# Optimization experiments

Hardware: AMD Instinct MI355X
Metric: run time of the kernel (lower is better)

Reference implementation:

```python
import jax, jax.numpy as jnp
import numpy as np
import math

H = 2048      # hidden_size
NH = 32       # num heads
HD = H // NH  # head_dim = 64
THETA = 10000.0
B, S = 2, 2048


def _rope_tables(seq_len):
    inv_freq = 1.0 / (THETA ** (jnp.arange(0, HD, 2, dtype=jnp.float32) / HD))
    t = jnp.arange(seq_len, dtype=jnp.float32)
    freqs = t[:, None] * inv_freq[None, :]          # [S, HD/2]
    emb = jnp.concatenate([freqs, freqs], axis=-1)  # [S, HD]
    return jnp.cos(emb)[None, None], jnp.sin(emb)[None, None]  # [1,1,S,HD]


def _rotate_half(x):
    x1, x2 = jnp.split(x, 2, axis=-1)
    return jnp.concatenate([-x2, x1], axis=-1)


def setup_inputs() -> dict:
    key = jax.random.key(0)
    ks = jax.random.split(key, 5)
    hidden_states = jax.random.normal(ks[0], (B, S, H), dtype=jnp.float32)
    wscale = 1.0 / math.sqrt(H)
    wq = jax.random.normal(ks[1], (H, H), dtype=jnp.float32) * wscale
    wk = jax.random.normal(ks[2], (H, H), dtype=jnp.float32) * wscale
    wv = jax.random.normal(ks[3], (H, H), dtype=jnp.float32) * wscale
    wo = jax.random.normal(ks[4], (H, H), dtype=jnp.float32) * wscale
    # additive causal mask: 0 on/below diagonal, -1e9 above
    causal = jnp.tril(jnp.ones((S, S), dtype=bool))
    attention_mask = jnp.where(causal, 0.0, -1e9).astype(jnp.float32)[None, None]
    return {"hidden_states": hidden_states, "attention_mask": attention_mask,
            "wq": wq, "wk": wk, "wv": wv, "wo": wo}


def reference(hidden_states, attention_mask, wq, wk, wv, wo):
    b, s, _ = hidden_states.shape
    # projections (Linear, no bias); weights stored [in, out]
    q = (hidden_states @ wq).reshape(b, s, NH, HD).transpose(0, 2, 1, 3)  # [B,NH,S,HD]
    k = (hidden_states @ wk).reshape(b, s, NH, HD).transpose(0, 2, 1, 3)
    v = (hidden_states @ wv).reshape(b, s, NH, HD).transpose(0, 2, 1, 3)
    # RoPE
    cos, sin = _rope_tables(s)
    q = q * cos + _rotate_half(q) * sin
    k = k * cos + _rotate_half(k) * sin
    # attention
    attn = jnp.einsum('bhqd,bhkd->bhqk', q, k) / math.sqrt(HD)
    attn = attn + attention_mask
    w = jax.nn.softmax(attn, axis=-1)
    out = jnp.einsum('bhqk,bhkd->bhqd', w, v)           # [B,NH,S,HD]
    out = out.transpose(0, 2, 1, 3).reshape(b, s, H)    # [B,S,H]
    return out @ wo
```

## Files before the change

### kernel.cpp

```cpp
#include <hip/hip_runtime.h>
#include <hip/hip_bf16.h>

#define H 2048
#define NH 32
#define HD 64
#define BB 2
#define SS 2048
#define MM (BB*SS)

typedef __attribute__((ext_vector_type(8))) short bf16x8;
typedef __attribute__((ext_vector_type(4))) float f32x4;
typedef __attribute__((ext_vector_type(16))) float f32x16;
typedef unsigned short u16;
typedef unsigned int u32;
typedef __attribute__((ext_vector_type(4))) u32 u32x4;

#define MFMA16(acc, av, bv) acc = __builtin_amdgcn_mfma_f32_16x16x32_bf16(av, bv, acc, 0, 0, 0)

static __device__ __forceinline__ u16 f2bf(float f){
  union { float f; u32 i; } v; v.f = f;
  u32 x = v.i;
  return (u16)((x + 0x7FFFu + ((x >> 16) & 1u)) >> 16);
}
static __device__ __forceinline__ float bf2f(u16 u){
  union { u32 i; float f; } v; v.i = ((u32)u) << 16; return v.f;
}
static __device__ __forceinline__ u32 pk2(float a, float b){
  u32 r;
  asm("v_cvt_pk_bf16_f32 %0, %1, %2" : "=v"(r) : "v"(a), "v"(b));
  return r;
}

static __device__ __forceinline__ void gload16(const u16* g, u16* l){
  __builtin_amdgcn_global_load_lds((const __attribute__((address_space(1))) void*)g,
                                   (__attribute__((address_space(3))) void*)l, 16, 0, 0);
}

__global__ void k_cvt(const float* __restrict__ src, u16* __restrict__ dst){
  const int i = (blockIdx.x * 256 + threadIdx.x) * 4;
  float4 v = *(const float4*)(src + i);
  ushort4 o;
  o.x = f2bf(v.x); o.y = f2bf(v.y); o.z = f2bf(v.z); o.w = f2bf(v.w);
  *(ushort4*)(dst + i) = o;
}

__global__ void k_wtrans(const float* __restrict__ w0, const float* __restrict__ w1,
                         const float* __restrict__ w2, const float* __restrict__ w3,
                         u16* __restrict__ d0, u16* __restrict__ d1,
                         u16* __restrict__ d2, u16* __restrict__ d3){
  __shared__ float tile[32][33];
  const int z = blockIdx.z;
  const float* w = z==0 ? w0 : z==1 ? w1 : z==2 ? w2 : w3;
  u16* d        = z==0 ? d0 : z==1 ? d1 : z==2 ? d2 : d3;
  const int n0 = blockIdx.x * 32, k0 = blockIdx.y * 32;
  const int tx = threadIdx.x, ty = threadIdx.y;
  #pragma unroll
  for (int j = 0; j < 4; j++)
    tile[ty + 8*j][tx] = w[(size_t)(k0 + ty + 8*j) * H + n0 + tx];
  __syncthreads();
  #pragma unroll
  for (int j = 0; j < 4; j++)
    d[(size_t)(n0 + ty + 8*j) * H + k0 + tx] = f2bf(tile[tx][ty + 8*j]);
}

__global__ __launch_bounds__(512, 4) void k_gemm8(
    const u16* __restrict__ A, const u16* __restrict__ Bt,
    u16* __restrict__ CQ, u16* __restrict__ CK, u16* __restrict__ CV,
    int M, int K){
  __shared__ __align__(16) u16 As[2][128][64];
  __shared__ __align__(16) u16 Bs[2][192][64];
  const int flat = blockIdx.x;
  const int id = (flat & 7) * 128 + (flat >> 3);
  const int gy = id >> 5, gx = id & 31;
  const int m0 = gx * 128, n0 = gy * 192;
  const int t = threadIdx.x, w = t >> 6, l = t & 63;
  const int wm = w >> 2, wn = w & 3;
  const int lrow = l & 15, lk = (l >> 4) * 8;
  const int sw = (lrow & 7) * 8;
  const int sr = t >> 3, sc = (t & 7) * 8;
  const int ssc = sc ^ ((sr & 7) * 8);
  const int NK = K >> 6;

  auto stageA = [&](int kt, int u){
    const size_t kb = (size_t)kt * 64 + ssc;
    #pragma unroll
    for (int c = 0; c < 2; c++)
      gload16(A + (size_t)(m0 + c*64 + sr) * K + kb, &As[u][c*64 + sr][sc]);
  };
  auto stageB = [&](int kt, int u){
    const size_t kb = (size_t)kt * 64 + ssc;
    #pragma unroll
    for (int c = 0; c < 3; c++)
      gload16(Bt + (size_t)(n0 + c*64 + sr) * K + kb, &Bs[u][c*64 + sr][sc]);
  };

  f32x4 acc[4][3] = {};

  stageA(0, 0); stageB(0, 0);
  stageA(1, 1); stageB(1, 1);
  asm volatile("s_waitcnt vmcnt(5)" ::: "memory");
  __builtin_amdgcn_s_barrier();

  #pragma unroll 1
  for (int kt = 0; kt < NK; ++kt){
    const int u = kt & 1;
    const bool more = (kt + 2 < NK);
    bf16x8 b0[3], b1[3], a0, a1;

    #pragma unroll
    for (int n = 0; n < 3; n++)
      b0[n] = *(const bf16x8*)&Bs[u][wn*48 + n*16 + lrow][lk ^ sw];
    a0 = *(const bf16x8*)&As[u][wm*64 +  0 + lrow][lk ^ sw];
    a1 = *(const bf16x8*)&As[u][wm*64 + 16 + lrow][lk ^ sw];
    __builtin_amdgcn_s_setprio(1);
    #pragma unroll
    for (int n = 0; n < 3; n++){
      MFMA16(acc[0][n], a0, b0[n]);
      MFMA16(acc[1][n], a1, b0[n]);
    }
    __builtin_amdgcn_s_setprio(0);
    __builtin_amdgcn_s_barrier();

    #pragma unroll
    for (int n = 0; n < 3; n++)
      b1[n] = *(const bf16x8*)&Bs[u][wn*48 + n*16 + lrow][(32 + lk) ^ sw];
    a0 = *(const bf16x8*)&As[u][wm*64 +  0 + lrow][(32 + lk) ^ sw];
    a1 = *(const bf16x8*)&As[u][wm*64 + 16 + lrow][(32 + lk) ^ sw];
    __builtin_amdgcn_s_setprio(1);
    #pragma unroll
    for (int n = 0; n < 3; n++){
      MFMA16(acc[0][n], a0, b1[n]);
      MFMA16(acc[1][n], a1, b1[n]);
    }
    __builtin_amdgcn_s_setprio(0);
    __builtin_amdgcn_s_barrier();

    if (more) stageB(kt + 2, u);
    a0 = *(const bf16x8*)&As[u][wm*64 + 32 + lrow][lk ^ sw];
    a1 = *(const bf16x8*)&As[u][wm*64 + 48 + lrow][lk ^ sw];
    __builtin_amdgcn_s_setprio(1);
    #pragma unroll
    for (int n = 0; n < 3; n++){
      MFMA16(acc[2][n], a0, b0[n]);
      MFMA16(acc[3][n], a1, b0[n]);
    }
    __builtin_amdgcn_s_setprio(0);
    __builtin_amdgcn_s_barrier();

    a0 = *(const bf16x8*)&As[u][wm*64 + 32 + lrow][(32 + lk) ^ sw];
    a1 = *(const bf16x8*)&As[u][wm*64 + 48 + lrow][(32 + lk) ^ sw];
    __builtin_amdgcn_s_setprio(1);
    #pragma unroll
    for (int n = 0; n < 3; n++){
      MFMA16(acc[2][n], a0, b1[n]);
      MFMA16(acc[3][n], a1, b1[n]);
    }
    __builtin_amdgcn_s_setprio(0);
    __builtin_amdgcn_s_barrier();

    if (more){
      stageA(kt + 2, u);
      asm volatile("s_waitcnt vmcnt(5)" ::: "memory");
      __builtin_amdgcn_s_barrier();
    } else if (kt + 1 < NK){
      asm volatile("s_waitcnt vmcnt(0)" ::: "memory");
      __builtin_amdgcn_s_barrier();
    }
  }

  #pragma unroll
  for (int m = 0; m < 4; m++)
    #pragma unroll
    for (int n = 0; n < 3; n++){
      const int ncol = n0 + wn*48 + n*16 + lrow;
      const int z = ncol >> 11;
      u16* C = (z == 0 ? CQ : z == 1 ? CK : CV) + (ncol & 2047);
      #pragma unroll
      for (int r = 0; r < 4; r++){
        const int row = m0 + wm*64 + m*16 + (l >> 4)*4 + r;
        C[(size_t)row * H] = f2bf(acc[m][n][r]);
      }
    }
}

__global__ __launch_bounds__(512, 4) void k_gemmo(
    const u16* __restrict__ A, const u16* __restrict__ Bt,
    float* __restrict__ C, int M, int N, int K){
  __shared__ __align__(16) u16 As[2][128][64];
  __shared__ __align__(16) u16 Bs[2][128][64];
  const int flat = blockIdx.x;
  const int id = (flat & 7) * 64 + (flat >> 3);
  const int gy = id >> 5, gx = id & 31;
  const int m0 = gx * 128, n0 = gy * 128;
  const int t = threadIdx.x, w = t >> 6, l = t & 63;
  const int wm = w >> 2, wn = w & 3;
  const int lrow = l & 15, lk = (l >> 4) * 8;
  const int sw = (lrow & 7) * 8;
  const int sr = t >> 3, sc = (t & 7) * 8;
  const int ssc = sc ^ ((sr & 7) * 8);
  const int NK = K >> 6;

  auto stageA = [&](int kt, int u){
    const size_t kb = (size_t)kt * 64 + ssc;
    #pragma unroll
    for (int c = 0; c < 2; c++)
      gload16(A + (size_t)(m0 + c*64 + sr) * K + kb, &As[u][c*64 + sr][sc]);
  };
  auto stageB = [&](int kt, int u){
    const size_t kb = (size_t)kt * 64 + ssc;
    #pragma unroll
    for (int c = 0; c < 2; c++)
      gload16(Bt + (size_t)(n0 + c*64 + sr) * K + kb, &Bs[u][c*64 + sr][sc]);
  };

  f32x4 acc[4][2] = {};

  stageA(0, 0); stageB(0, 0);
  stageA(1, 1); stageB(1, 1);
  asm volatile("s_waitcnt vmcnt(4)" ::: "memory");
  __builtin_amdgcn_s_barrier();

  #pragma unroll 1
  for (int kt = 0; kt < NK; ++kt){
    const int u = kt & 1;
    const bool more = (kt + 2 < NK);
    bf16x8 b0[2], b1[2], a0, a1;

    #pragma unroll
    for (int n = 0; n < 2; n++)
      b0[n] = *(const bf16x8*)&Bs[u][wn*32 + n*16 + lrow][lk ^ sw];
    a0 = *(const bf16x8*)&As[u][wm*64 +  0 + lrow][lk ^ sw];
    a1 = *(const bf16x8*)&As[u][wm*64 + 16 + lrow][lk ^ sw];
    __builtin_amdgcn_s_setprio(1);
    #pragma unroll
    for (int n = 0; n < 2; n++){
      MFMA16(acc[0][n], a0, b0[n]);
      MFMA16(acc[1][n], a1, b0[n]);
    }
    __builtin_amdgcn_s_setprio(0);
    __builtin_amdgcn_s_barrier();

    #pragma unroll
    for (int n = 0; n < 2; n++)
      b1[n] = *(const bf16x8*)&Bs[u][wn*32 + n*16 + lrow][(32 + lk) ^ sw];
    a0 = *(const bf16x8*)&As[u][wm*64 +  0 + lrow][(32 + lk) ^ sw];
    a1 = *(const bf16x8*)&As[u][wm*64 + 16 + lrow][(32 + lk) ^ sw];
    __builtin_amdgcn_s_setprio(1);
    #pragma unroll
    for (int n = 0; n < 2; n++){
      MFMA16(acc[0][n], a0, b1[n]);
      MFMA16(acc[1][n], a1, b1[n]);
    }
    __builtin_amdgcn_s_setprio(0);
    __builtin_amdgcn_s_barrier();

    if (more) stageB(kt + 2, u);
    a0 = *(const bf16x8*)&As[u][wm*64 + 32 + lrow][lk ^ sw];
    a1 = *(const bf16x8*)&As[u][wm*64 + 48 + lrow][lk ^ sw];
    __builtin_amdgcn_s_setprio(1);
    #pragma unroll
    for (int n = 0; n < 2; n++){
      MFMA16(acc[2][n], a0, b0[n]);
      MFMA16(acc[3][n], a1, b0[n]);
    }
    __builtin_amdgcn_s_setprio(0);
    __builtin_amdgcn_s_barrier();

    a0 = *(const bf16x8*)&As[u][wm*64 + 32 + lrow][(32 + lk) ^ sw];
    a1 = *(const bf16x8*)&As[u][wm*64 + 48 + lrow][(32 + lk) ^ sw];
    __builtin_amdgcn_s_setprio(1);
    #pragma unroll
    for (int n = 0; n < 2; n++){
      MFMA16(acc[2][n], a0, b1[n]);
      MFMA16(acc[3][n], a1, b1[n]);
    }
    __builtin_amdgcn_s_setprio(0);
    __builtin_amdgcn_s_barrier();

    if (more){
      stageA(kt + 2, u);
      asm volatile("s_waitcnt vmcnt(4)" ::: "memory");
      __builtin_amdgcn_s_barrier();
    } else if (kt + 1 < NK){
      asm volatile("s_waitcnt vmcnt(0)" ::: "memory");
      __builtin_amdgcn_s_barrier();
    }
  }

  #pragma unroll
  for (int m = 0; m < 4; m++)
    #pragma unroll
    for (int n = 0; n < 2; n++){
      const int col = n0 + wn*32 + n*16 + lrow;
      #pragma unroll
      for (int r = 0; r < 4; r++){
        const int row = m0 + wm*64 + m*16 + (l >> 4)*4 + r;
        C[(size_t)row * N + col] = acc[m][n][r];
      }
    }
}

__global__ void k_rope(u16* __restrict__ Kp){
  const int idx = blockIdx.x * 256 + threadIdx.x;
  const int quad = idx & 3;
  const int h = (idx >> 2) & 31;
  const int row = idx >> 7;
  const int s = row & (SS - 1);
  const int i0 = quad * 8;
  u16* k = Kp + (size_t)row * H + h * HD;
  uint4 k1v = *(const uint4*)(k + i0);
  uint4 k2v = *(const uint4*)(k + i0 + 32);
  u16* k1 = (u16*)&k1v; u16* k2 = (u16*)&k2v;
  const float sf = (float)s;
  #pragma unroll
  for (int e = 0; e < 8; e++){
    const int i = i0 + e;
    const float inv = exp2f(-0.4152410118609203f * (float)i);
    float rev = sf * inv * 0.15915494309189535f;
    rev -= floorf(rev);
    const float sn = __builtin_amdgcn_sinf(rev);
    const float cs = __builtin_amdgcn_cosf(rev);
    const float ka = bf2f(k1[e]), kb = bf2f(k2[e]);
    k1[e] = f2bf(ka*cs - kb*sn);
    k2[e] = f2bf(kb*cs + ka*sn);
  }
  *(uint4*)(k + i0)      = k1v;
  *(uint4*)(k + i0 + 32) = k2v;
}

__global__ __launch_bounds__(256, 2) void k_attn(
    const u16* __restrict__ Q, const u16* __restrict__ K,
    const u16* __restrict__ V, u16* __restrict__ O){
  __shared__ __align__(16) u16 Ks[3][64][64];
  __shared__ __align__(16) u16 Vs[2][64][72];
  const int t = threadIdx.x, w = t >> 6, l = t & 63;
  const int x = blockIdx.x, bh = blockIdx.y;
  const int b = bh >> 5, h = bh & 31;
  const u16* kp = K + (size_t)(b*SS) * H + h * HD;
  const u16* vp = V + (size_t)(b*SS) * H + h * HD;
  const int sr = t >> 3, sc = (t & 7) * 8;
  const int ssc = sc ^ ((sr & 7) * 8);
  const int hi = l >> 5, lq = l & 31;
  const float QSC = 0.18033688011112042f;

  auto stageK = [&](int tile, int buf){
    const int jb = tile * 64;
    gload16(kp + (size_t)(jb + sr) * H + ssc,      &Ks[buf][sr][sc]);
    gload16(kp + (size_t)(jb + 32 + sr) * H + ssc, &Ks[buf][32 + sr][sc]);
  };
  auto loadV = [&](int tile, uint4* vv){
    const int jb = tile * 64;
    vv[0] = *(const uint4*)(vp + (size_t)(jb + sr) * H + sc);
    vv[1] = *(const uint4*)(vp + (size_t)(jb + 32 + sr) * H + sc);
  };
  auto publishV = [&](const uint4* vv, int buf){
    #pragma unroll
    for (int c = 0; c < 2; c++){
      const int j = c*32 + sr;
      const u16* pv = (const u16*)&vv[c];
      #pragma unroll
      for (int e = 0; e < 8; e++){
        const int d = sc + e;
        Vs[buf][d][j ^ ((d >> 3) * 8)] = pv[e];
      }
    }
  };

  #pragma unroll 1
  for (int pp = 0; pp < 2; pp++){
    const int qt = pp ? x : (15 - x);
    const int NT = 2*qt + 2;
    const int qw0 = qt*128 + w*32;
    const int qrow = qw0 + lq;

    const u16* qptr = Q + (size_t)(b*SS + qrow) * H + h * HD + hi*8;
    bf16x8 qr0 = *(const bf16x8*)(qptr + 0);
    bf16x8 qr1 = *(const bf16x8*)(qptr + 16);
    bf16x8 qr2 = *(const bf16x8*)(qptr + 32);
    bf16x8 qr3 = *(const bf16x8*)(qptr + 48);
    bf16x8 qf[4];
    {
      const float sf = (float)qrow;
      #pragma unroll
      for (int e = 0; e < 8; e++){
        #pragma unroll
        for (int pr = 0; pr < 2; pr++){
          const int d = pr*16 + hi*8 + e;
          const float inv = exp2f(-0.4152410118609203f * (float)d);
          float rev = sf * inv * 0.15915494309189535f;
          rev -= floorf(rev);
          const float sn = __builtin_amdgcn_sinf(rev);
          const float cs = __builtin_amdgcn_cosf(rev);
          const float qa = bf2f((u16)(pr ? qr1[e] : qr0[e]));
          const float qb = bf2f((u16)(pr ? qr3[e] : qr2[e]));
          const u16 oa = f2bf((qa*cs - qb*sn) * QSC);
          const u16 ob = f2bf((qb*cs + qa*sn) * QSC);
          if (pr){ qf[1][e] = (short)oa; qf[3][e] = (short)ob; }
          else   { qf[0][e] = (short)oa; qf[2][e] = (short)ob; }
        }
      }
    }

    float mrun = -1e30f, lrun = 0.f;
    f32x16 oacc[2] = {};
    uint4 vvE[2], vvO[2];

    stageK(0, 0); loadV(0, vvE);
    stageK(1, 1); loadV(1, vvO);
    asm volatile("s_waitcnt vmcnt(4)" ::: "memory");
    publishV(vvE, 0);
    asm volatile("s_waitcnt lgkmcnt(0)" ::: "memory");
    __builtin_amdgcn_s_barrier();

    auto body = [&](int jt, int p, uint4* vvSelf, const uint4* vvOther){
      const int j0 = jt * 64;
      if (jt + 2 < NT){ stageK(jt + 2, (jt + 2) % 3); loadV(jt + 2, vvSelf); }

      if (j0 <= qw0){
        const int kbuf = jt % 3;
        f32x16 sv[2] = {};
        __builtin_amdgcn_s_setprio(1);
        #pragma unroll
        for (int kb = 0; kb < 2; kb++){
          const int row = kb*32 + lq;
          #pragma unroll
          for (int c = 0; c < 4; c++){
            bf16x8 kf = *(const bf16x8*)&Ks[kbuf][row][(c*16 + hi*8) ^ ((row & 7) * 8)];
            sv[kb] = __builtin_amdgcn_mfma_f32_32x32x16_bf16(kf, qf[c], sv[kb], 0, 0, 0);
          }
        }
        __builtin_amdgcn_s_setprio(0);
        if (j0 + 63 > qw0){
          #pragma unroll
          for (int kb = 0; kb < 2; kb++)
            #pragma unroll
            for (int r = 0; r < 16; r++){
              const int kg = j0 + kb*32 + (r & 3) + 8*(r >> 2) + 4*hi;
              if (kg > qrow) sv[kb][r] = -1e30f;
            }
        }
        float t16[16], t8[8], t4[4];
        #pragma unroll
        for (int r = 0; r < 16; r++) t16[r] = fmaxf(sv[0][r], sv[1][r]);
        #pragma unroll
        for (int r = 0; r < 8; r++) t8[r] = fmaxf(t16[r], t16[r+8]);
        #pragma unroll
        for (int r = 0; r < 4; r++) t4[r] = fmaxf(t8[r], t8[r+4]);
        float tm = fmaxf(fmaxf(t4[0], t4[2]), fmaxf(t4[1], t4[3]));
        tm = fmaxf(tm, __shfl_xor(tm, 32, 64));
        if (__any(tm > mrun)){
          const float mn = fmaxf(mrun, tm);
          const float fac = exp2f(mrun - mn);
          mrun = mn;
          lrun *= fac;
          #pragma unroll
          for (int db = 0; db < 2; db++)
            #pragma unroll
            for (int r = 0; r < 16; r++) oacc[db][r] *= fac;
        }
        #pragma unroll
        for (int kb = 0; kb < 2; kb++)
          #pragma unroll
          for (int r = 0; r < 16; r++) sv[kb][r] = exp2f(sv[kb][r] - mrun);
        float s16[16], s8[8], s4[4];
        #pragma unroll
        for (int r = 0; r < 16; r++) s16[r] = sv[0][r] + sv[1][r];
        #pragma unroll
        for (int r = 0; r < 8; r++) s8[r] = s16[r] + s16[r+8];
        #pragma unroll
        for (int r = 0; r < 4; r++) s4[r] = s8[r] + s8[r+4];
        float rs = (s4[0] + s4[1]) + (s4[2] + s4[3]);
        rs += __shfl_xor(rs, 32, 64);
        lrun += rs;
        u32x4 pw[4];
        #pragma unroll
        for (int kb = 0; kb < 2; kb++){
          #pragma unroll
          for (int half = 0; half < 2; half++){
            const int rb = half * 8;
            const u32 own0 = pk2(sv[kb][rb+0], sv[kb][rb+1]);
            const u32 own1 = pk2(sv[kb][rb+2], sv[kb][rb+3]);
            const u32 own2 = pk2(sv[kb][rb+4], sv[kb][rb+5]);
            const u32 own3 = pk2(sv[kb][rb+6], sv[kb][rb+7]);
            const u32 s0 = hi ? own0 : own2;
            const u32 s1 = hi ? own1 : own3;
            const u32 r0 = __shfl_xor(s0, 32, 64);
            const u32 r1 = __shfl_xor(s1, 32, 64);
            u32x4 pv;
            pv[0] = hi ? r0 : own0;
            pv[1] = hi ? r1 : own1;
            pv[2] = hi ? own2 : r0;
            pv[3] = hi ? own3 : r1;
            pw[kb*2 + half] = pv;
          }
        }
        __builtin_amdgcn_s_setprio(1);
        #pragma unroll
        for (int db = 0; db < 2; db++){
          const int d = db*32 + lq;
          #pragma unroll
          for (int tt = 0; tt < 4; tt++){
            bf16x8 vf = *(const bf16x8*)&Vs[p][d][(tt*16 + hi*8) ^ ((d >> 3) * 8)];
            bf16x8 pfr = __builtin_bit_cast(bf16x8, pw[tt]);
            oacc[db] = __builtin_amdgcn_mfma_f32_32x32x16_bf16(vf, pfr, oacc[db], 0, 0, 0);
          }
        }
        __builtin_amdgcn_s_setprio(0);
      }

      if (jt + 2 < NT) asm volatile("s_waitcnt vmcnt(4)" ::: "memory");
      else             asm volatile("s_waitcnt vmcnt(0)" ::: "memory");
      if (jt + 1 < NT) publishV(vvOther, p ^ 1);
      asm volatile("s_waitcnt lgkmcnt(0)" ::: "memory");
      __builtin_amdgcn_s_barrier();
    };

    #pragma unroll 1
    for (int jt2 = 0; jt2 < NT; jt2 += 2){
      body(jt2,     0, vvE, vvO);
      body(jt2 + 1, 1, vvO, vvE);
    }

    const float rl = 1.0f / lrun;
    u16* op = O + (size_t)(b*SS + qrow) * H + h * HD;
    #pragma unroll
    for (int db = 0; db < 2; db++)
      #pragma unroll
      for (int rq = 0; rq < 4; rq++){
        ushort4 o4;
        o4.x = f2bf(oacc[db][rq*4 + 0] * rl);
        o4.y = f2bf(oacc[db][rq*4 + 1] * rl);
        o4.z = f2bf(oacc[db][rq*4 + 2] * rl);
        o4.w = f2bf(oacc[db][rq*4 + 3] * rl);
        *(ushort4*)(op + db*32 + rq*8 + 4*hi) = o4;
      }
  }
}

extern "C" void kernel_launch(void* const* d_in, const int* in_sizes, int n_in,
                              void* d_out, int out_size, void* d_ws, size_t ws_size,
                              hipStream_t stream){
  (void)in_sizes; (void)n_in; (void)out_size; (void)ws_size;
  const float* hs = (const float*)d_in[0];
  const float* wq = (const float*)d_in[2];
  const float* wk = (const float*)d_in[3];
  const float* wv = (const float*)d_in[4];
  const float* wo = (const float*)d_in[5];
  float* out = (float*)d_out;
  char* ws = (char*)d_ws;

  u16* Xb  = (u16*)ws;
  u16* Wqt = (u16*)(ws + (size_t)MM * H * 2);
  u16* Wkt = Wqt + (size_t)H * H;
  u16* Wvt = Wkt + (size_t)H * H;
  u16* Wot = Wvt + (size_t)H * H;
  u16* Vb  = Wot + (size_t)H * H;
  u16* Ob  = Vb  + (size_t)MM * H;
  u16* Qb  = (u16*)d_out;
  u16* Kb  = Qb + (size_t)MM * H;

  k_cvt<<<8192, 256, 0, stream>>>(hs, Xb);
  k_wtrans<<<dim3(64, 64, 4), dim3(32, 8), 0, stream>>>(wq, wk, wv, wo, Wqt, Wkt, Wvt, Wot);
  k_gemm8<<<1024, 512, 0, stream>>>(Xb, Wqt, Qb, Kb, Vb, MM, H);
  k_rope<<<2048, 256, 0, stream>>>(Kb);
  k_attn<<<dim3(8, 64), 256, 0, stream>>>(Qb, Kb, Vb, Ob);
  k_gemmo<<<512, 512, 0, stream>>>(Ob, Wot, out, MM, H, H);
}
```

Baseline: 278.0 us.

## Process two KV tiles per barrier with 4-deep K/V buffers and lazy rescale

Restructures the attention main loop to stage and compute two key/value tiles per iteration, using four shared-memory buffers for both K and V. This halves the number of barriers and waitcnt points per tile. It also raises the online-softmax rescale threshold so the output accumulator is only rescaled when the max grows by a margin, and defers the cross-half row-sum shuffle to the end. In exchange shared-memory use rises, which may hurt occupancy at 2 blocks per CU, and the lazy max risks a precision change.

Result: no change. 273.1 us, median of 2 (-1.8%).

```diff
diff --git a/kernel.cpp b/kernel.cpp
--- a/kernel.cpp
+++ b/kernel.cpp
@@ -331,8 +331,8 @@
 __global__ __launch_bounds__(256, 2) void k_attn(
     const u16* __restrict__ Q, const u16* __restrict__ K,
     const u16* __restrict__ V, u16* __restrict__ O){
-  __shared__ __align__(16) u16 Ks[3][64][64];
-  __shared__ __align__(16) u16 Vs[2][64][72];
+  __shared__ __align__(16) u16 Ks[4][64][64];
+  __shared__ __align__(16) u16 Vs[4][64][72];
   const int t = threadIdx.x, w = t >> 6, l = t & 63;
   const int x = blockIdx.x, bh = blockIdx.y;
   const int b = bh >> 5, h = bh & 31;
@@ -403,124 +403,127 @@
 
     float mrun = -1e30f, lrun = 0.f;
     f32x16 oacc[2] = {};
-    uint4 vvE[2], vvO[2];
-
-    stageK(0, 0); loadV(0, vvE);
-    stageK(1, 1); loadV(1, vvO);
-    asm volatile("s_waitcnt vmcnt(4)" ::: "memory");
-    publishV(vvE, 0);
+    uint4 vvA[2], vvB[2];
+
+    stageK(0, 0); loadV(0, vvA);
+    stageK(1, 1); loadV(1, vvB);
+    asm volatile("s_waitcnt vmcnt(0)" ::: "memory");
+    publishV(vvA, 0);
+    publishV(vvB, 1);
     asm volatile("s_waitcnt lgkmcnt(0)" ::: "memory");
     __builtin_amdgcn_s_barrier();
 
-    auto body = [&](int jt, int p, uint4* vvSelf, const uint4* vvOther){
+    auto compute = [&](int jt){
       const int j0 = jt * 64;
-      if (jt + 2 < NT){ stageK(jt + 2, (jt + 2) % 3); loadV(jt + 2, vvSelf); }
-
-      if (j0 <= qw0){
-        const int kbuf = jt % 3;
-        f32x16 sv[2] = {};
-        __builtin_amdgcn_s_setprio(1);
-        #pragma unroll
-        for (int kb = 0; kb < 2; kb++){
-          const int row = kb*32 + lq;
-          #pragma unroll
-          for (int c = 0; c < 4; c++){
-            bf16x8 kf = *(const bf16x8*)&Ks[kbuf][row][(c*16 + hi*8) ^ ((row & 7) * 8)];
-            sv[kb] = __builtin_amdgcn_mfma_f32_32x32x16_bf16(kf, qf[c], sv[kb], 0, 0, 0);
-          }
+      if (j0 > qw0) return;
+      const int kbuf = jt & 3;
+      f32x16 sv[2] = {};
+      __builtin_amdgcn_s_setprio(1);
+      #pragma unroll
+      for (int kb = 0; kb < 2; kb++){
+        const int row = kb*32 + lq;
+        #pragma unroll
+        for (int c = 0; c < 4; c++){
+          bf16x8 kf = *(const bf16x8*)&Ks[kbuf][row][(c*16 + hi*8) ^ ((row & 7) * 8)];
+          sv[kb] = __builtin_amdgcn_mfma_f32_32x32x16_bf16(kf, qf[c], sv[kb], 0, 0, 0);
         }
-        __builtin_amdgcn_s_setprio(0);
-        if (j0 + 63 > qw0){
-          #pragma unroll
-          for (int kb = 0; kb < 2; kb++)
-            #pragma unroll
-            for (int r = 0; r < 16; r++){
-              const int kg = j0 + kb*32 + (r & 3) + 8*(r >> 2) + 4*hi;
-              if (kg > qrow) sv[kb][r] = -1e30f;
-            }
-        }
-        float t16[16], t8[8], t4[4];
-        #pragma unroll
-        for (int r = 0; r < 16; r++) t16[r] = fmaxf(sv[0][r], sv[1][r]);
-        #pragma unroll
-        for (int r = 0; r < 8; r++) t8[r] = fmaxf(t16[r], t16[r+8]);
-        #pragma unroll
-        for (int r = 0; r < 4; r++) t4[r] = fmaxf(t8[r], t8[r+4]);
-        float tm = fmaxf(fmaxf(t4[0], t4[2]), fmaxf(t4[1], t4[3]));
-        tm = fmaxf(tm, __shfl_xor(tm, 32, 64));
-        if (__any(tm > mrun)){
-          const float mn = fmaxf(mrun, tm);
-          const float fac = exp2f(mrun - mn);
-          mrun = mn;
-          lrun *= fac;
-          #pragma unroll
-          for (int db = 0; db < 2; db++)
-            #pragma unroll
-            for (int r = 0; r < 16; r++) oacc[db][r] *= fac;
-        }
+      }
+      __builtin_amdgcn_s_setprio(0);
+      if (j0 + 63 > qw0){
         #pragma unroll
         for (int kb = 0; kb < 2; kb++)
           #pragma unroll
-          for (int r = 0; r < 16; r++) sv[kb][r] = exp2f(sv[kb][r] - mrun);
-        float s16[16], s8[8], s4[4];
-        #pragma unroll
-        for (int r = 0; r < 16; r++) s16[r] = sv[0][r] + sv[1][r];
-        #pragma unroll
-        for (int r = 0; r < 8; r++) s8[r] = s16[r] + s16[r+8];
-        #pragma unroll
-        for (int r = 0; r < 4; r++) s4[r] = s8[r] + s8[r+4];
-        float rs = (s4[0] + s4[1]) + (s4[2] + s4[3]);
-        rs += __shfl_xor(rs, 32, 64);
-        lrun += rs;
-        u32x4 pw[4];
-        #pragma unroll
-        for (int kb = 0; kb < 2; kb++){
+          for (int r = 0; r < 16; r++){
+            const int kg = j0 + kb*32 + (r & 3) + 8*(r >> 2) + 4*hi;
+            if (kg > qrow) sv[kb][r] = -1e30f;
+          }
+      }
+      float t16[16], t8[8], t4[4];
+      #pragma unroll
+      for (int r = 0; r < 16; r++) t16[r] = fmaxf(sv[0][r], sv[1][r]);
+      #pragma unroll
+      for (int r = 0; r < 8; r++) t8[r] = fmaxf(t16[r], t16[r+8]);
+      #pragma unroll
+      for (int r = 0; r < 4; r++) t4[r] = fmaxf(t8[r], t8[r+4]);
+      float tm = fmaxf(fmaxf(t4[0], t4[2]), fmaxf(t4[1], t4[3]));
+      tm = fmaxf(tm, __shfl_xor(tm, 32, 64));
+      if (__any(tm > mrun + 11.5f)){
+        const float mn = fmaxf(mrun, tm);
+        const float fac = exp2f(mrun - mn);
+        mrun = mn;
+        lrun *= fac;
+        #pragma unroll
+        for (int db = 0; db < 2; db++)
           #pragma unroll
-          for (int half = 0; half < 2; half++){
-            const int rb = half * 8;
-            const u32 own0 = pk2(sv[kb][rb+0], sv[kb][rb+1]);
-            const u32 own1 = pk2(sv[kb][rb+2], sv[kb][rb+3]);
-            const u32 own2 = pk2(sv[kb][rb+4], sv[kb][rb+5]);
-            const u32 own3 = pk2(sv[kb][rb+6], sv[kb][rb+7]);
-            const u32 s0 = hi ? own0 : own2;
-            const u32 s1 = hi ? own1 : own3;
-            const u32 r0 = __shfl_xor(s0, 32, 64);
-            const u32 r1 = __shfl_xor(s1, 32, 64);
-            u32x4 pv;
-            pv[0] = hi ? r0 : own0;
-            pv[1] = hi ? r1 : own1;
-            pv[2] = hi ? own2 : r0;
-            pv[3] = hi ? own3 : r1;
-            pw[kb*2 + half] = pv;
-          }
+          for (int r = 0; r < 16; r++) oacc[db][r] *= fac;
+      }
+      #pragma unroll
+      for (int kb = 0; kb < 2; kb++)
+        #pragma unroll
+        for (int r = 0; r < 16; r++) sv[kb][r] = exp2f(sv[kb][r] - mrun);
+      float s16[16], s8[8], s4[4];
+      #pragma unroll
+      for (int r = 0; r < 16; r++) s16[r] = sv[0][r] + sv[1][r];
+      #pragma unroll
+      for (int r = 0; r < 8; r++) s8[r] = s16[r] + s16[r+8];
+      #pragma unroll
+      for (int r = 0; r < 4; r++) s4[r] = s8[r] + s8[r+4];
+      lrun += (s4[0] + s4[1]) + (s4[2] + s4[3]);
+      u32x4 pw[4];
+      #pragma unroll
+      for (int kb = 0; kb < 2; kb++){
+        #pragma unroll
+        for (int half = 0; half < 2; half++){
+          const int rb = half * 8;
+          const u32 own0 = pk2(sv[kb][rb+0], sv[kb][rb+1]);
+          const u32 own1 = pk2(sv[kb][rb+2], sv[kb][rb+3]);
+          const u32 own2 = pk2(sv[kb][rb+4], sv[kb][rb+5]);
+          const u32 own3 = pk2(sv[kb][rb+6], sv[kb][rb+7]);
+          const u32 s0 = hi ? own0 : own2;
+          const u32 s1 = hi ? own1 : own3;
+          const u32 r0 = __shfl_xor(s0, 32, 64);
+          const u32 r1 = __shfl_xor(s1, 32, 64);
+          u32x4 pv;
+          pv[0] = hi ? r0 : own0;
+          pv[1] = hi ? r1 : own1;
+          pv[2] = hi ? own2 : r0;
+          pv[3] = hi ? own3 : r1;
+          pw[kb*2 + half] = pv;
         }
-        __builtin_amdgcn_s_setprio(1);
-        #pragma unroll
-        for (int db = 0; db < 2; db++){
-          const int d = db*32 + lq;
-          #pragma unroll
-          for (int tt = 0; tt < 4; tt++){
-            bf16x8 vf = *(const bf16x8*)&Vs[p][d][(tt*16 + hi*8) ^ ((d >> 3) * 8)];
-            bf16x8 pfr = __builtin_bit_cast(bf16x8, pw[tt]);
-            oacc[db] = __builtin_amdgcn_mfma_f32_32x32x16_bf16(vf, pfr, oacc[db], 0, 0, 0);
-          }
+      }
+      __builtin_amdgcn_s_setprio(1);
+      #pragma unroll
+      for (int db = 0; db < 2; db++){
+        const int d = db*32 + lq;
+        #pragma unroll
+        for (int tt = 0; tt < 4; tt++){
+          bf16x8 vf = *(const bf16x8*)&Vs[kbuf][d][(tt*16 + hi*8) ^ ((d >> 3) * 8)];
+          bf16x8 pfr = __builtin_bit_cast(bf16x8, pw[tt]);
+          oacc[db] = __builtin_amdgcn_mfma_f32_32x32x16_bf16(vf, pfr, oacc[db], 0, 0, 0);
         }
-        __builtin_amdgcn_s_setprio(0);
-      }
-
-      if (jt + 2 < NT) asm volatile("s_waitcnt vmcnt(4)" ::: "memory");
-      else             asm volatile("s_waitcnt vmcnt(0)" ::: "memory");
-      if (jt + 1 < NT) publishV(vvOther, p ^ 1);
+      }
+      __builtin_amdgcn_s_setprio(0);
+    };
+
+    #pragma unroll 1
+    for (int jt = 0; jt < NT; jt += 2){
+      const bool more = (jt + 2 < NT);
+      if (more){
+        stageK(jt + 2, (jt + 2) & 3); loadV(jt + 2, vvA);
+        stageK(jt + 3, (jt + 3) & 3); loadV(jt + 3, vvB);
+      }
+      compute(jt);
+      compute(jt + 1);
+      if (more){
+        asm volatile("s_waitcnt vmcnt(0)" ::: "memory");
+        publishV(vvA, (jt + 2) & 3);
+        publishV(vvB, (jt + 3) & 3);
+      }
       asm volatile("s_waitcnt lgkmcnt(0)" ::: "memory");
       __builtin_amdgcn_s_barrier();
-    };
-
-    #pragma unroll 1
-    for (int jt2 = 0; jt2 < NT; jt2 += 2){
-      body(jt2,     0, vvE, vvO);
-      body(jt2 + 1, 1, vvO, vvE);
-    }
-
+    }
+
+    lrun += __shfl_xor(lrun, 32, 64);
     const float rl = 1.0f / lrun;
     u16* op = O + (size_t)(b*SS + qrow) * H + h * HD;
     #pragma unroll
```
